# Kernel tuning notes

Measured on AMD Instinct MI355X. Metric: run time of the kernel, lower is better.

## Reference

```python
import jax, jax.numpy as jnp
import numpy as np

KP_EXTENT = 1.2  # influence radius of each kernel point (init arg KP_extent)
SHADOW_COORD = 1e6  # shadow point coordinate for padding (as in original KPConv)


def setup_inputs() -> dict:
    key = jax.random.key(0)
    k1, k2, k3, k4, k5, k6 = jax.random.split(key, 6)
    N, Ns, H, K, Cin, Cout = 20000, 20000, 40, 15, 128, 128
    q_pts = jax.random.uniform(k1, (N, 3), dtype=jnp.float32)
    s_pts = jax.random.uniform(k2, (Ns, 3), dtype=jnp.float32)
    neighb_inds = jax.random.randint(k3, (N, H), 0, Ns, dtype=jnp.int32)
    x = jax.random.normal(k4, (Ns, Cin), dtype=jnp.float32)
    # kernel point positions inside the sphere (stand-in for load_kernels output)
    kernel_points = jax.random.normal(k5, (K, 3), dtype=jnp.float32) * 0.5
    kernel_points = kernel_points.at[0].set(0.0)  # fixed='center'
    weights = jax.random.normal(k6, (K, Cin, Cout), dtype=jnp.float32) * (1.0 / np.sqrt(Cin))
    return {"q_pts": q_pts, "s_pts": s_pts, "neighb_inds": neighb_inds,
            "x": x, "kernel_points": kernel_points, "weights": weights}


def reference(q_pts, s_pts, neighb_inds, x, kernel_points, weights):
    # Pad support points with a far-away shadow point and features with a zero row,
    # so out-of-range neighbor index Ns contributes nothing (original KPConv trick).
    s_pad = jnp.concatenate([s_pts, jnp.full((1, s_pts.shape[1]), SHADOW_COORD, s_pts.dtype)], axis=0)
    x_pad = jnp.concatenate([x, jnp.zeros((1, x.shape[1]), x.dtype)], axis=0)

    # Gather neighbor coords, center on query points: [N, H, 3]
    neighbors = s_pad[neighb_inds] - q_pts[:, None, :]

    # Squared distance to every kernel point: [N, H, K]
    diff = neighbors[:, :, None, :] - kernel_points[None, None, :, :]
    sq_dist = jnp.sum(diff * diff, axis=-1)

    # Linear influence weights, aggregation_mode='sum': [N, K, H]
    all_weights = jnp.clip(1.0 - jnp.sqrt(sq_dist) / KP_EXTENT, 0.0, None)
    all_weights = jnp.swapaxes(all_weights, 1, 2)

    # Gather neighbor features: [N, H, Cin]
    neighb_x = x_pad[neighb_inds]

    # Influence-weighted aggregation over neighbors: [N, K, Cin]
    weighted = jnp.einsum('nkh,nhc->nkc', all_weights, neighb_x)

    # Per-kernel-point linear maps, summed over kernel points: [N, Cout]
    out = jnp.einsum('nkc,kcd->nd', weighted, weights)
    return out
```

## Files before the change

### kernel.cpp

```cpp
#include <hip/hip_runtime.h>

#define KP   15
#define HN   40
#define CIN  128
#define COUT 128
#define KDIM (KP*CIN)
#define KP_EXT_INV (1.0f/1.2f)
#define AM   16
#define GBM  32
#define GBK  128

typedef __bf16 bf16x8 __attribute__((ext_vector_type(8)));
typedef __bf16 bf16x4 __attribute__((ext_vector_type(4)));
typedef float  f32x4  __attribute__((ext_vector_type(4)));

__device__ inline void async_copy16(const void* g, void* lds) {
    __builtin_amdgcn_global_load_lds(
        (const __attribute__((address_space(1))) unsigned int*)g,
        (__attribute__((address_space(3))) unsigned int*)lds, 16, 0, 0);
}
#define LGKM0() __asm__ __volatile__("s_waitcnt lgkmcnt(0)" ::: "memory")

__global__ __launch_bounds__(256)
void kpconv_prep(const float* __restrict__ x, const float* __restrict__ W,
                 __bf16* __restrict__ xb, __bf16* __restrict__ Wt,
                 int nx_elems, int nxB)
{
    __shared__ float sW[32][133];
    const int b = blockIdx.x;
    const int t = threadIdx.x;

    if (b < nxB) {
        const int e0 = (b*256 + t) * 8;
        if (e0 + 8 <= nx_elems) {
            const float4 f0 = *(const float4*)(x + e0);
            const float4 f1 = *(const float4*)(x + e0 + 4);
            bf16x8 v;
            v[0]=(__bf16)f0.x; v[1]=(__bf16)f0.y; v[2]=(__bf16)f0.z; v[3]=(__bf16)f0.w;
            v[4]=(__bf16)f1.x; v[5]=(__bf16)f1.y; v[6]=(__bf16)f1.z; v[7]=(__bf16)f1.w;
            *(bf16x8*)(xb + e0) = v;
        } else {
            for (int e = e0; e < nx_elems; ++e) xb[e] = (__bf16)x[e];
        }
    } else {
        const int kc0 = (b - nxB) * 32;
        #pragma unroll
        for (int i = 0; i < 4; ++i) {
            const int off = t*4 + i*1024;
            const int r = off >> 7, c = off & 127;
            const float4 f = *(const float4*)(W + (size_t)(kc0 + r)*COUT + c);
            sW[r][c+0]=f.x; sW[r][c+1]=f.y; sW[r][c+2]=f.z; sW[r][c+3]=f.w;
        }
        __syncthreads();
        #pragma unroll
        for (int i = 0; i < 2; ++i) {
            const int id = t + i*256;
            const int d  = id >> 2, ch = id & 3;
            bf16x8 v;
            #pragma unroll
            for (int j = 0; j < 8; ++j) v[j] = (__bf16)sW[ch*8 + j][d];
            *(bf16x8*)(Wt + (size_t)d*KDIM + kc0 + ch*8) = v;
        }
    }
}

struct alignas(16) SharedA {
    __bf16 sXt[4][4][128][8];
    float4 s_nd[4][2][HN];
    int    s_idx[4][2][HN];
};

__global__ __launch_bounds__(256, 4)
void kpconv_phaseA(const float* __restrict__ q_pts,
                   const float* __restrict__ s_pts,
                   const int*   __restrict__ nb,
                   const __bf16* __restrict__ xb,
                   const float* __restrict__ kpts,
                   __bf16* __restrict__ wsA,
                   int N, int Ns)
{
    __shared__ SharedA sh;

    const int t  = threadIdx.x;
    const int wv = t >> 6;
    const int l  = t & 63;
    const int m  = l & 15;
    const int q  = l >> 4;
    const int m0 = blockIdx.x * AM;

    float kx=0.f, ky=0.f, kz=0.f;
    if (m < KP) { kx = kpts[m*3+0]; ky = kpts[m*3+1]; kz = kpts[m*3+2]; }
    const float kk  = kx*kx + ky*ky + kz*kz;
    const float kx2 = -2.f*kx, ky2 = -2.f*ky, kz2 = -2.f*kz;

    {
        const int n0 = m0 + wv*4;
        if (l < HN) {
            int idx = nb[n0*HN + l];
            float dx, dy, dz;
            if (idx >= 0 && idx < Ns) {
                dx = s_pts[idx*3+0] - q_pts[n0*3+0];
                dy = s_pts[idx*3+1] - q_pts[n0*3+1];
                dz = s_pts[idx*3+2] - q_pts[n0*3+2];
            } else { idx = 0; dx = dy = dz = 2.0e6f; }
            sh.s_idx[wv][0][l] = idx;
            sh.s_nd[wv][0][l]  = make_float4(dx, dy, dz, dx*dx+dy*dy+dz*dz);
        }
        LGKM0();
    }

    uint4 g[5][2];
    #pragma unroll
    for (int itx = 0; itx < 5; ++itx) {
        const int h0 = (itx < 4) ? (itx*8 + 2*q) : (32 + 2*q);
        g[itx][0] = *(const uint4*)(xb + (size_t)sh.s_idx[wv][0][h0  ]*CIN + m*8);
        g[itx][1] = *(const uint4*)(xb + (size_t)sh.s_idx[wv][0][h0+1]*CIN + m*8);
    }

    for (int pi = 0; pi < 4; ++pi) {
        const int cur = pi & 1;
        const int nxt = cur ^ 1;
        const int n   = m0 + wv*4 + pi;
        const bool hasNext = (pi < 3);

        int   p_idx = 0;
        float p_dx = 2.0e6f, p_dy = 2.0e6f, p_dz = 2.0e6f;
        if (hasNext && l < HN) {
            const int n1 = n + 1;
            int idx = nb[n1*HN + l];
            if (idx >= 0 && idx < Ns) {
                p_idx = idx;
                p_dx = s_pts[idx*3+0] - q_pts[n1*3+0];
                p_dy = s_pts[idx*3+1] - q_pts[n1*3+1];
                p_dz = s_pts[idx*3+2] - q_pts[n1*3+2];
            }
        }

        bf16x8 wfrag[2];
        #pragma unroll
        for (int ks = 0; ks < 2; ++ks) {
            #pragma unroll
            for (int j = 0; j < 8; ++j) {
                const int h = ks*32 + q*8 + j;
                float w = 0.f;
                if (m < KP && h < HN) {
                    const float4 nd = sh.s_nd[wv][cur][h];
                    const float d2 = fmaf(nd.x, kx2,
                                     fmaf(nd.y, ky2,
                                     fmaf(nd.z, kz2, nd.w + kk)));
                    const float d = __builtin_amdgcn_sqrtf(d2);
                    w = fmaxf(fmaf(d, -KP_EXT_INV, 1.0f), 0.f);
                }
                wfrag[ks][j] = (__bf16)w;
            }
        }

        f32x4 acc[8];
        #pragma unroll
        for (int nt = 0; nt < 8; ++nt) acc[nt] = (f32x4){0.f,0.f,0.f,0.f};

        #pragma unroll
        for (int itx = 0; itx < 4; ++itx) {
            const unsigned av[4] = {g[itx][0].x, g[itx][0].y, g[itx][0].z, g[itx][0].w};
            const unsigned bv[4] = {g[itx][1].x, g[itx][1].y, g[itx][1].z, g[itx][1].w};
            unsigned* plane = (unsigned*)&sh.sXt[wv][itx][0][0];
            #pragma unroll
            for (int j = 0; j < 8; ++j) {
                const unsigned v = __builtin_amdgcn_perm(
                    bv[j>>1], av[j>>1], (j&1) ? 0x07060302u : 0x05040100u);
                const int p = m*8 + (j ^ (m & 7));
                plane[p*4 + q] = v;
            }
        }
        LGKM0();
        #pragma unroll
        for (int nt = 0; nt < 8; ++nt) {
            const int cc = nt*16 + m;
            const int p  = (cc & ~7) | ((cc & 7) ^ ((cc >> 3) & 7));
            bf16x8 xf = *(const bf16x8*)&sh.sXt[wv][q][p][0];
            acc[nt] = __builtin_amdgcn_mfma_f32_16x16x32_bf16(
                          xf, wfrag[0], acc[nt], 0, 0, 0);
        }

        {
            const unsigned av[4] = {g[4][0].x, g[4][0].y, g[4][0].z, g[4][0].w};
            const unsigned bv[4] = {g[4][1].x, g[4][1].y, g[4][1].z, g[4][1].w};
            unsigned* plane = (unsigned*)&sh.sXt[wv][0][0][0];
            #pragma unroll
            for (int j = 0; j < 8; ++j) {
                const unsigned v = __builtin_amdgcn_perm(
                    bv[j>>1], av[j>>1], (j&1) ? 0x07060302u : 0x05040100u);
                const int p = m*8 + (j ^ (m & 7));
                plane[p*4 + q] = v;
            }
        }

        if (hasNext) {
            if (l < HN) {
                sh.s_idx[wv][nxt][l] = p_idx;
                sh.s_nd[wv][nxt][l]  = make_float4(p_dx, p_dy, p_dz,
                                                   p_dx*p_dx + p_dy*p_dy + p_dz*p_dz);
            }
            LGKM0();
            #pragma unroll
            for (int itx = 0; itx < 5; ++itx) {
                const int h0 = (itx < 4) ? (itx*8 + 2*q) : (32 + 2*q);
                g[itx][0] = *(const uint4*)(xb + (size_t)sh.s_idx[wv][nxt][h0  ]*CIN + m*8);
                g[itx][1] = *(const uint4*)(xb + (size_t)sh.s_idx[wv][nxt][h0+1]*CIN + m*8);
            }
        }

        LGKM0();
        #pragma unroll
        for (int nt = 0; nt < 8; ++nt) {
            const int cc = nt*16 + m;
            const int p  = (cc & ~7) | ((cc & 7) ^ ((cc >> 3) & 7));
            bf16x8 xf = *(const bf16x8*)&sh.sXt[wv][q][p][0];
            acc[nt] = __builtin_amdgcn_mfma_f32_16x16x32_bf16(
                          xf, wfrag[1], acc[nt], 0, 0, 0);
        }

        if (m < KP) {
            #pragma unroll
            for (int nt = 0; nt < 8; ++nt) {
                bf16x4 v;
                #pragma unroll
                for (int r = 0; r < 4; ++r) v[r] = (__bf16)acc[nt][r];
                *(bf16x4*)(wsA + (size_t)n*KDIM + m*CIN + nt*16 + q*4) = v;
            }
        }
    }
}

struct alignas(16) SharedB { __bf16 sA[GBM*GBK]; __bf16 sB[COUT*GBK]; };

__global__ __launch_bounds__(256, 4)
void kpconv_gemm(const __bf16* __restrict__ wsA,
                 const __bf16* __restrict__ Wt,
                 float* __restrict__ out, int N)
{
    __shared__ SharedB sh;

    const int t  = threadIdx.x;
    const int wv = t >> 6;
    const int l  = t & 63;
    const int m  = l & 15;
    const int q  = l >> 4;
    const int m0 = blockIdx.x * GBM;
    const int rA = t >> 4;
    const int pA = t & 15;

    f32x4 acc[2][2];
    #pragma unroll
    for (int i = 0; i < 2; ++i)
        #pragma unroll
        for (int j = 0; j < 2; ++j) acc[i][j] = (f32x4){0.f,0.f,0.f,0.f};

    for (int k0 = 0; k0 < KDIM; k0 += GBK) {
        #pragma unroll
        for (int pass = 0; pass < 2; ++pass) {
            const int r  = rA + pass*16;
            const int ch = pA ^ (r & 15);
            async_copy16(wsA + (size_t)(m0 + r)*KDIM + k0 + ch*8,
                         (char*)sh.sA + pass*4096 + wv*1024 + l*16);
        }
        #pragma unroll
        for (int pass = 0; pass < 8; ++pass) {
            const int r  = rA + pass*16;
            const int ch = pA ^ (r & 15);
            async_copy16(Wt + (size_t)r*KDIM + k0 + ch*8,
                         (char*)sh.sB + pass*4096 + wv*1024 + l*16);
        }
        __syncthreads();

        #pragma unroll
        for (int ks = 0; ks < 4; ++ks) {
            bf16x8 af[2], bfr[2];
            #pragma unroll
            for (int mt = 0; mt < 2; ++mt) {
                const int row = mt*16 + m;
                const int p   = (ks*4 + q) ^ (row & 15);
                af[mt] = *(const bf16x8*)&sh.sA[row*GBK + p*8];
            }
            #pragma unroll
            for (int j = 0; j < 2; ++j) {
                const int row = (wv*2 + j)*16 + m;
                const int p   = (ks*4 + q) ^ (row & 15);
                bfr[j] = *(const bf16x8*)&sh.sB[row*GBK + p*8];
            }
            #pragma unroll
            for (int mt = 0; mt < 2; ++mt)
                #pragma unroll
                for (int j = 0; j < 2; ++j)
                    acc[mt][j] = __builtin_amdgcn_mfma_f32_16x16x32_bf16(
                                     af[mt], bfr[j], acc[mt][j], 0, 0, 0);
        }
        __syncthreads();
    }

    #pragma unroll
    for (int mt = 0; mt < 2; ++mt)
        #pragma unroll
        for (int j = 0; j < 2; ++j)
            #pragma unroll
            for (int r = 0; r < 4; ++r)
                out[(size_t)(m0 + mt*16 + q*4 + r)*COUT
                    + (wv*2+j)*16 + m] = acc[mt][j][r];
}

#define TM 8
#define WSTR (KP*CIN + 4)

__global__ __launch_bounds__(256, 2)
void kpconv_fused(const float* __restrict__ q_pts,
                  const float* __restrict__ s_pts,
                  const int*   __restrict__ nb,
                  const float* __restrict__ x,
                  const float* __restrict__ kpts,
                  const float* __restrict__ W,
                  float* __restrict__ out,
                  int N, int Ns)
{
    __shared__ float s_kp[KP*3];
    __shared__ float s_nd2[HN*3];
    __shared__ int   s_idx2[HN];
    __shared__ float s_w[KP][HN];
    __shared__ float s_wt[TM*WSTR];

    const int t  = threadIdx.x;
    const int n0 = (int)blockIdx.x * TM;
    if (t < KP*3) s_kp[t] = kpts[t];
    const int c = t & (CIN-1);
    const int g = t >> 7;

    for (int mm = 0; mm < TM; ++mm) {
        const int n = n0 + mm;
        if (t < HN) {
            float dx = 1e6f, dy = 1e6f, dz = 1e6f;
            int idx = 0;
            if (n < N) {
                idx = nb[n*HN + t];
                if (idx >= 0 && idx < Ns) {
                    dx = s_pts[idx*3+0] - q_pts[n*3+0];
                    dy = s_pts[idx*3+1] - q_pts[n*3+1];
                    dz = s_pts[idx*3+2] - q_pts[n*3+2];
                } else idx = 0;
            }
            s_idx2[t] = idx;
            s_nd2[t*3+0] = dx; s_nd2[t*3+1] = dy; s_nd2[t*3+2] = dz;
        }
        __syncthreads();
        for (int task = t; task < KP*HN; task += 256) {
            const int k = task / HN;
            const int h = task - k*HN;
            const float dx = s_nd2[h*3+0] - s_kp[k*3+0];
            const float dy = s_nd2[h*3+1] - s_kp[k*3+1];
            const float dz = s_nd2[h*3+2] - s_kp[k*3+2];
            s_w[k][h] = fmaxf(1.0f - sqrtf(dx*dx+dy*dy+dz*dz)*KP_EXT_INV, 0.0f);
        }
        __syncthreads();
        float facc[8];
        #pragma unroll
        for (int j = 0; j < 8; ++j) facc[j] = 0.0f;
        #pragma unroll 8
        for (int h = 0; h < HN; ++h) {
            const float xv = x[s_idx2[h]*CIN + c];
            #pragma unroll
            for (int j = 0; j < 8; ++j) {
                const int k = g + 2*j;
                if (k < KP) facc[j] += s_w[k][h] * xv;
            }
        }
        #pragma unroll
        for (int j = 0; j < 8; ++j) {
            const int k = g + 2*j;
            if (k < KP) s_wt[mm*WSTR + k*CIN + c] = facc[j];
        }
        __syncthreads();
    }

    const int m3 = t >> 5;
    const int d0 = (t & 31) * 4;
    const float* wm = &s_wt[m3*WSTR];
    float ax = 0.f, ay = 0.f, az = 0.f, aw = 0.f;
    #pragma unroll 4
    for (int kc = 0; kc < KP*CIN; ++kc) {
        const float  wvv = wm[kc];
        const float4 wr = *(const float4*)&W[kc*COUT + d0];
        ax += wvv * wr.x; ay += wvv * wr.y; az += wvv * wr.z; aw += wvv * wr.w;
    }
    const int n = n0 + m3;
    if (n < N) {
        float4 o; o.x = ax; o.y = ay; o.z = az; o.w = aw;
        *(float4*)&out[n*COUT + d0] = o;
    }
}

extern "C" void kernel_launch(void* const* d_in, const int* in_sizes, int n_in,
                              void* d_out, int out_size, void* d_ws, size_t ws_size,
                              hipStream_t stream) {
    const float* q_pts = (const float*)d_in[0];
    const float* s_pts = (const float*)d_in[1];
    const int*   nb    = (const int*)  d_in[2];
    const float* x     = (const float*)d_in[3];
    const float* kpts  = (const float*)d_in[4];
    const float* W     = (const float*)d_in[5];
    float* out = (float*)d_out;

    const int N  = in_sizes[0] / 3;
    const int Ns = in_sizes[1] / 3;
    const int nx = in_sizes[3];

    const size_t needA = (size_t)N * KDIM * sizeof(__bf16);
    const size_t needB = (size_t)COUT * KDIM * sizeof(__bf16);
    const size_t needX = (size_t)nx * sizeof(__bf16);

    if (ws_size >= needA + needB + needX && (N % GBM) == 0 && (nx % 8) == 0
        && (KDIM % GBK) == 0) {
        __bf16* wsA = (__bf16*)d_ws;
        __bf16* wsB = (__bf16*)((char*)d_ws + needA);
        __bf16* wsX = (__bf16*)((char*)d_ws + needA + needB);

        const int nxB = (nx/8 + 255) / 256;
        const int nwB = KDIM / 32;
        hipLaunchKernelGGL(kpconv_prep, dim3(nxB + nwB), dim3(256), 0, stream,
                           x, W, wsX, wsB, nx, nxB);
        hipLaunchKernelGGL(kpconv_phaseA, dim3(N/AM), dim3(256), 0, stream,
                           q_pts, s_pts, nb, wsX, kpts, wsA, N, Ns);
        hipLaunchKernelGGL(kpconv_gemm, dim3(N/GBM), dim3(256), 0, stream,
                           wsA, wsB, out, N);
    } else {
        const int grid = (N + TM - 1) / TM;
        hipLaunchKernelGGL(kpconv_fused, dim3(grid), dim3(256), 0, stream,
                           q_pts, s_pts, nb, x, kpts, W, out, N, Ns);
    }
}
```

Measured before the change: 145.7 us.

## Permute K dimension to store wide phase-A outputs and raise rows per block

Phase A now writes each accumulator pair as a single 16-byte store instead of two 8-byte stores. To allow this, the K dimension of the intermediate is permuted, and the weight-prep kernel builds the transposed weights with the same permutation, gathering directly from global memory without the LDS transpose. Each phase-A block now handles 20 query points (5 per wave) instead of 16, which cuts block count and amortizes the per-block setup. The point-coordinate loads are also merged into float3 reads. The risks are the uncoalesced strided reads in the prep kernel and the added N%20 requirement for the fast path.

```diff
diff --git a/kernel.cpp b/kernel.cpp
--- a/kernel.cpp
+++ b/kernel.cpp
@@ -6,7 +6,7 @@
 #define COUT 128
 #define KDIM (KP*CIN)
 #define KP_EXT_INV (1.0f/1.2f)
-#define AM   16
+#define AM   20
 #define GBM  32
 #define GBK  128
 
@@ -20,13 +20,13 @@
         (__attribute__((address_space(3))) unsigned int*)lds, 16, 0, 0);
 }
 #define LGKM0() __asm__ __volatile__("s_waitcnt lgkmcnt(0)" ::: "memory")
+
 
 __global__ __launch_bounds__(256)
 void kpconv_prep(const float* __restrict__ x, const float* __restrict__ W,
                  __bf16* __restrict__ xb, __bf16* __restrict__ Wt,
                  int nx_elems, int nxB)
 {
-    __shared__ float sW[32][133];
     const int b = blockIdx.x;
     const int t = threadIdx.x;
 
@@ -43,24 +43,21 @@
             for (int e = e0; e < nx_elems; ++e) xb[e] = (__bf16)x[e];
         }
     } else {
-        const int kc0 = (b - nxB) * 32;
-        #pragma unroll
-        for (int i = 0; i < 4; ++i) {
-            const int off = t*4 + i*1024;
-            const int r = off >> 7, c = off & 127;
-            const float4 f = *(const float4*)(W + (size_t)(kc0 + r)*COUT + c);
-            sW[r][c+0]=f.x; sW[r][c+1]=f.y; sW[r][c+2]=f.z; sW[r][c+3]=f.w;
-        }
-        __syncthreads();
-        #pragma unroll
-        for (int i = 0; i < 2; ++i) {
-            const int id = t + i*256;
-            const int d  = id >> 2, ch = id & 3;
-            bf16x8 v;
-            #pragma unroll
-            for (int j = 0; j < 8; ++j) v[j] = (__bf16)sW[ch*8 + j][d];
-            *(bf16x8*)(Wt + (size_t)d*KDIM + kc0 + ch*8) = v;
-        }
+        const int gid = (b - nxB)*256 + t;
+        const int gr  = gid >> 7;
+        const int d   = gid & 127;
+        bf16x8 v;
+        #pragma unroll
+        for (int j = 0; j < 8; ++j) {
+            const int kcp = gr*8 + j;
+            const int mm = kcp >> 7;
+            const int qq = (kcp >> 5) & 3;
+            const int nt = (kcp >> 2) & 7;
+            const int rr = kcp & 3;
+            const int kc = mm*128 + nt*16 + qq*4 + rr;
+            v[j] = (__bf16)W[(size_t)kc*COUT + d];
+        }
+        *(bf16x8*)(Wt + (size_t)d*KDIM + gr*8) = v;
     }
 }
 
@@ -94,14 +91,14 @@
     const float kx2 = -2.f*kx, ky2 = -2.f*ky, kz2 = -2.f*kz;
 
     {
-        const int n0 = m0 + wv*4;
+        const int n0 = m0 + wv*5;
         if (l < HN) {
             int idx = nb[n0*HN + l];
             float dx, dy, dz;
             if (idx >= 0 && idx < Ns) {
-                dx = s_pts[idx*3+0] - q_pts[n0*3+0];
-                dy = s_pts[idx*3+1] - q_pts[n0*3+1];
-                dz = s_pts[idx*3+2] - q_pts[n0*3+2];
+                const float3 sp = *(const float3*)(s_pts + (size_t)idx*3);
+                const float3 qp = *(const float3*)(q_pts + (size_t)n0*3);
+                dx = sp.x - qp.x; dy = sp.y - qp.y; dz = sp.z - qp.z;
             } else { idx = 0; dx = dy = dz = 2.0e6f; }
             sh.s_idx[wv][0][l] = idx;
             sh.s_nd[wv][0][l]  = make_float4(dx, dy, dz, dx*dx+dy*dy+dz*dz);
@@ -117,11 +114,11 @@
         g[itx][1] = *(const uint4*)(xb + (size_t)sh.s_idx[wv][0][h0+1]*CIN + m*8);
     }
 
-    for (int pi = 0; pi < 4; ++pi) {
+    for (int pi = 0; pi < 5; ++pi) {
         const int cur = pi & 1;
         const int nxt = cur ^ 1;
-        const int n   = m0 + wv*4 + pi;
-        const bool hasNext = (pi < 3);
+        const int n   = m0 + wv*5 + pi;
+        const bool hasNext = (pi < 4);
 
         int   p_idx = 0;
         float p_dx = 2.0e6f, p_dy = 2.0e6f, p_dz = 2.0e6f;
@@ -130,9 +127,9 @@
             int idx = nb[n1*HN + l];
             if (idx >= 0 && idx < Ns) {
                 p_idx = idx;
-                p_dx = s_pts[idx*3+0] - q_pts[n1*3+0];
-                p_dy = s_pts[idx*3+1] - q_pts[n1*3+1];
-                p_dz = s_pts[idx*3+2] - q_pts[n1*3+2];
+                const float3 sp = *(const float3*)(s_pts + (size_t)idx*3);
+                const float3 qp = *(const float3*)(q_pts + (size_t)n1*3);
+                p_dx = sp.x - qp.x; p_dy = sp.y - qp.y; p_dz = sp.z - qp.z;
             }
         }
 
@@ -222,11 +219,14 @@
 
         if (m < KP) {
             #pragma unroll
-            for (int nt = 0; nt < 8; ++nt) {
-                bf16x4 v;
+            for (int s = 0; s < 4; ++s) {
+                bf16x8 v;
                 #pragma unroll
-                for (int r = 0; r < 4; ++r) v[r] = (__bf16)acc[nt][r];
-                *(bf16x4*)(wsA + (size_t)n*KDIM + m*CIN + nt*16 + q*4) = v;
+                for (int r = 0; r < 4; ++r) {
+                    v[r]   = (__bf16)acc[2*s  ][r];
+                    v[4+r] = (__bf16)acc[2*s+1][r];
+                }
+                *(bf16x8*)(wsA + (size_t)n*KDIM + m*128 + q*32 + s*8) = v;
             }
         }
     }
@@ -415,14 +415,14 @@
     const size_t needB = (size_t)COUT * KDIM * sizeof(__bf16);
     const size_t needX = (size_t)nx * sizeof(__bf16);
 
-    if (ws_size >= needA + needB + needX && (N % GBM) == 0 && (nx % 8) == 0
-        && (KDIM % GBK) == 0) {
+    if (ws_size >= needA + needB + needX && (N % GBM) == 0 && (N % AM) == 0
+        && (nx % 8) == 0 && (KDIM % GBK) == 0) {
         __bf16* wsA = (__bf16*)d_ws;
         __bf16* wsB = (__bf16*)((char*)d_ws + needA);
         __bf16* wsX = (__bf16*)((char*)d_ws + needA + needB);
 
         const int nxB = (nx/8 + 255) / 256;
-        const int nwB = KDIM / 32;
+        const int nwB = (KDIM * COUT / 8) / 256;
         hipLaunchKernelGGL(kpconv_prep, dim3(nxB + nwB), dim3(256), 0, stream,
                            x, W, wsX, wsB, nx, nxB);
         hipLaunchKernelGGL(kpconv_phaseA, dim3(N/AM), dim3(256), 0, stream,
```

New measurement: 139.3 us. -4.4%, faster.
